# Kernel tuning notes

Measured on AMD Instinct MI355X. Metric: run time of the kernel, lower is better.

Reference implementation:

```python
import jax, jax.numpy as jnp
import numpy as np

WS = 8          # window size
HEADS = 3       # num_heads
DIM = 48        # channels


def _rel_pos_log(ws):
    # log-spaced relative coordinates, (N, N, 2) with N = ws*ws
    coords = jnp.stack(jnp.meshgrid(jnp.arange(ws), jnp.arange(ws), indexing='ij'))  # (2, ws, ws)
    cf = coords.reshape(2, -1)                                  # (2, N)
    rel = (cf[:, :, None] - cf[:, None, :]).transpose(1, 2, 0)  # (N, N, 2)
    rel = rel.astype(jnp.float32)
    return jnp.sign(rel) * jnp.log1p(jnp.abs(rel))


def setup_inputs() -> dict:
    key = jax.random.key(0)
    ks = jax.random.split(key, 11)
    s = 0.05  # keep pre-softmax logits in a sane range
    return {
        'X': jax.random.normal(ks[0], (2, DIM, 512, 512), jnp.float32),
        'v_w': jax.random.normal(ks[1], (DIM, DIM), jnp.float32) * s,
        'v_b': jnp.zeros((DIM,), jnp.float32),
        'qk_w': jax.random.normal(ks[2], (2 * DIM, DIM), jnp.float32) * s,
        'qk_b': jnp.zeros((2 * DIM,), jnp.float32),
        'proj_w': jax.random.normal(ks[3], (DIM, DIM), jnp.float32) * s,
        'proj_b': jnp.zeros((DIM,), jnp.float32),
        'meta1_w': jax.random.normal(ks[4], (256, 2), jnp.float32) * s,
        'meta1_b': jnp.zeros((256,), jnp.float32),
        'meta2_w': jax.random.normal(ks[5], (HEADS, 256), jnp.float32) * s,
        'meta2_b': jnp.zeros((HEADS,), jnp.float32),
    }


def _conv1x1(x, w, b):
    # x: [B, Cin, H, W], w: [Cout, Cin], b: [Cout]
    return jnp.einsum('oc,bchw->bohw', w, x) + b[None, :, None, None]


def reference(X, v_w, v_b, qk_w, qk_b, proj_w, proj_b,
              meta1_w, meta1_b, meta2_w, meta2_b):
    B, C, H, W = X.shape
    hd = C // HEADS
    scale = hd ** -0.5
    N = WS * WS

    V = _conv1x1(X, v_w, v_b)              # [B, C, H, W]
    QK = _conv1x1(X, qk_w, qk_b)           # [B, 2C, H, W]
    QKV = jnp.concatenate([QK, V], axis=1)  # [B, 3C, H, W]

    # window partition (shift=0, H/W multiples of WS -> no padding)
    nh, nw = H // WS, W // WS
    x = QKV.transpose(0, 2, 3, 1)                           # [B, H, W, 3C]
    x = x.reshape(B, nh, WS, nw, WS, 3 * C)
    x = x.transpose(0, 1, 3, 2, 4, 5).reshape(B * nh * nw, N, 3 * C)

    qkv = x.reshape(-1, N, 3, HEADS, hd).transpose(2, 0, 3, 1, 4)  # [3, B_, h, N, d]
    q, k, v = qkv[0], qkv[1], qkv[2]

    attn = jnp.einsum('bhnd,bhmd->bhnm', q * scale, k)       # [B_, h, N, N]

    # MLP relative position bias
    rel = _rel_pos_log(WS)                                   # [N, N, 2]
    hidden = jax.nn.relu(rel @ meta1_w.T + meta1_b)          # [N, N, 256]
    bias = (hidden @ meta2_w.T + meta2_b).transpose(2, 0, 1)  # [h, N, N]

    attn = jax.nn.softmax(attn + bias[None], axis=-1)
    out = jnp.einsum('bhnm,bhmd->bhnd', attn, v)             # [B_, h, N, d]
    out = out.transpose(0, 2, 1, 3).reshape(B * nh * nw, N, C)

    # window reverse
    out = out.reshape(B, nh, nw, WS, WS, C)
    out = out.transpose(0, 1, 3, 2, 4, 5).reshape(B, H, W, C)
    out = out.transpose(0, 3, 1, 2)                          # [B, C, H, W]

    return _conv1x1(out, proj_w, proj_b)
```

## Files before the change

### kernel.cpp

```cpp
#include <hip/hip_runtime.h>
#include <math.h>


typedef _Float16 f16x4 __attribute__((ext_vector_type(4)));
typedef float    f32x4 __attribute__((ext_vector_type(4)));

#define WS_BFRAG 0
#define WS_WFRAG 49152
#define WS_PFRAG 62976
#define WS_QKVB  67584
#define WS_PBIAS 68160

#define XT_S 52
#define T_S  100
#define VD_S 68

__global__ __launch_bounds__(256) void prep_kernel(
    const float* __restrict__ m1w, const float* __restrict__ m1b,
    const float* __restrict__ m2w, const float* __restrict__ m2b,
    const float* __restrict__ qk_w, const float* __restrict__ v_w,
    const float* __restrict__ proj_w,
    const float* __restrict__ qk_b, const float* __restrict__ v_b,
    const float* __restrict__ proj_b,
    unsigned char* __restrict__ ws)
{
    __shared__ float sm[1536];

    float*     bfrag = (float*)(ws + WS_BFRAG);
    _Float16*  wfrag = (_Float16*)(ws + WS_WFRAG);
    _Float16*  pfrag = (_Float16*)(ws + WS_PFRAG);
    float*     qkvb  = (float*)(ws + WS_QKVB);
    float*     pbias = (float*)(ws + WS_PBIAS);

    const int gid = blockIdx.x * 256 + threadIdx.x;
    if (blockIdx.x < 16) {
        for (int i = threadIdx.x; i < 1536; i += 256) {
            float v;
            if (i < 512)      v = m1w[i];
            else if (i < 768) v = m1b[i - 512];
            else              v = m2w[i - 768];
            sm[i] = v;
        }
        __syncthreads();

        const int n = gid >> 6, m = gid & 63;
        float di = (float)((n >> 3) - (m >> 3));
        float dj = (float)((n & 7) - (m & 7));
        float r0 = copysignf(log1pf(fabsf(di)), di);
        float r1 = copysignf(log1pf(fabsf(dj)), dj);
        float a0 = 0.f, a1 = 0.f, a2 = 0.f;
        #pragma unroll 4
        for (int k = 0; k < 256; ++k) {
            float hv = fmaxf(sm[512 + k] + sm[2*k]*r0 + sm[2*k+1]*r1, 0.f);
            a0 += sm[768 + k]  * hv;
            a1 += sm[1024 + k] * hv;
            a2 += sm[1280 + k] * hv;
        }
        const int tm = m >> 4, quad = (m >> 2) & 3, r = m & 3, tn = n >> 4;
        const int ln = quad*16 + (n & 15);
        const int base = ((tm*4 + tn)*64 + ln)*4 + r;
        bfrag[(0*16*64)*4  + base] = a0 + m2b[0];
        bfrag[(16*64)*4    + base] = a1 + m2b[1];
        bfrag[(32*64)*4    + base] = a2 + m2b[2];
    } else if (gid < 4096 + 6912) {
        const int idx = gid - 4096;
        const int j = idx & 3, l = (idx >> 2) & 63, f = idx >> 8;
        const int ks = f % 3, mt = f / 3;
        const int row = mt*16 + (l & 15), col = ks*16 + ((l >> 4) << 2) + j;
        const float wv = (row < 96) ? qk_w[row*48 + col] : v_w[(row-96)*48 + col];
        wfrag[idx] = (_Float16)wv;
    } else if (gid < 11008 + 2304) {
        const int idx = gid - 11008;
        const int j = idx & 3, l = (idx >> 2) & 63, f = idx >> 8;
        const int ks = f % 3, mt = f / 3;
        const int row = mt*16 + (l & 15), col = ks*16 + ((l >> 4) << 2) + j;
        pfrag[idx] = (_Float16)proj_w[row*48 + col];
    } else if (gid < 13312 + 144) {
        const int c = gid - 13312;
        qkvb[c] = (c < 96) ? qk_b[c] : v_b[c - 96];
    } else if (gid < 13456 + 48) {
        pbias[gid - 13456] = proj_b[gid - 13456];
    }
}

__global__ __launch_bounds__(256, 4) void win_attn_kernel(
    const float* __restrict__ X, const unsigned char* __restrict__ ws,
    float* __restrict__ out, int nblk)
{
    __shared__ _Float16 smem[12992];
    _Float16* sXO = smem;
    _Float16* sT  = smem + 64*XT_S;
    _Float16* sVd = smem + 64*XT_S + 64*T_S;

    const float* bfrag = (const float*)(ws + WS_BFRAG);
    const f16x4* wfrag = (const f16x4*)(ws + WS_WFRAG);
    const f16x4* pfrag = (const f16x4*)(ws + WS_PFRAG);
    const float* qkvb  = (const float*)(ws + WS_QKVB);
    const float* pbias = (const float*)(ws + WS_PBIAS);

    const int tid  = threadIdx.x;
    const int wave = tid >> 6, lane = tid & 63;
    const int lq   = lane >> 4, lm = lane & 15;

    const int blk = blockIdx.x;
    const int wid = (blk & 7) * (nblk >> 3) + (blk >> 3);
    const int batch = wid >> 12;
    const int wh = (wid >> 6) & 63, ww = wid & 63;
    const int h0 = wh << 3, w0 = ww << 3;

    const float* Xb = X + ((size_t)batch * 48 << 18);

    f32x4 xv[3];
    #pragma unroll
    for (int g = 0; g < 3; ++g) {
        const int f = tid*12 + g*4;
        const int c = f >> 6, rw = (f >> 3) & 7, cl = f & 7;
        xv[g] = *(const f32x4*)(Xb + ((size_t)c << 18) + (size_t)(h0 + rw)*512 + (w0 + cl));
    }
    f16x4 aw[27];
    #pragma unroll
    for (int fi = 0; fi < 27; ++fi) aw[fi] = wfrag[fi*64 + lane];
    #pragma unroll
    for (int g = 0; g < 3; ++g) {
        const int f = tid*12 + g*4;
        const int c = f >> 6, rw = (f >> 3) & 7, cl = f & 7;
        #pragma unroll
        for (int j = 0; j < 4; ++j)
            sXO[(rw*8 + cl + j)*XT_S + c] = (_Float16)xv[g][j];
    }
    __syncthreads();

    {
        f16x4 bx[3];
        #pragma unroll
        for (int ks = 0; ks < 3; ++ks)
            bx[ks] = *(const f16x4*)&sXO[(wave*16 + lm)*XT_S + ks*16 + lq*4];

        const int tok = wave*16 + lm;
        #pragma unroll
        for (int mt = 0; mt < 9; ++mt) {
            f32x4 acc = *(const f32x4*)&qkvb[mt*16 + lq*4];
            #pragma unroll
            for (int ks = 0; ks < 3; ++ks)
                acc = __builtin_amdgcn_mfma_f32_16x16x16f16(aw[mt*3+ks], bx[ks], acc, 0, 0, 0);
            if (mt < 3) {
                f16x4 hv;
                #pragma unroll
                for (int r = 0; r < 4; ++r) hv[r] = (_Float16)(acc[r] * 0.25f);
                *(f16x4*)&sT[tok*T_S + mt*16 + lq*4] = hv;
            } else if (mt < 6) {
                f16x4 hv;
                #pragma unroll
                for (int r = 0; r < 4; ++r) hv[r] = (_Float16)acc[r];
                *(f16x4*)&sT[tok*T_S + mt*16 + lq*4] = hv;
            } else {
                #pragma unroll
                for (int r = 0; r < 4; ++r)
                    sVd[((mt-6)*16 + lq*4 + r)*VD_S + tok] = (_Float16)acc[r];
            }
        }
    }

    const int tn = wave;
    f32x4 sb[3][4];
    #pragma unroll
    for (int h = 0; h < 3; ++h)
        #pragma unroll
        for (int tm = 0; tm < 4; ++tm)
            sb[h][tm] = ((const f32x4*)bfrag)[(h*16 + tm*4 + tn)*64 + lane];
    __syncthreads();

    #pragma unroll
    for (int h = 0; h < 3; ++h) {
        f16x4 ak[4];
        #pragma unroll
        for (int tm = 0; tm < 4; ++tm)
            ak[tm] = *(const f16x4*)&sT[(tm*16 + lm)*T_S + 48 + h*16 + lq*4];
        f16x4 bq = *(const f16x4*)&sT[(tn*16 + lm)*T_S + h*16 + lq*4];
        f32x4 s[4];
        #pragma unroll
        for (int tm = 0; tm < 4; ++tm)
            s[tm] = __builtin_amdgcn_mfma_f32_16x16x16f16(ak[tm], bq, sb[h][tm], 0, 0, 0);

        float sum = 0.f;
        #pragma unroll
        for (int tm = 0; tm < 4; ++tm)
            #pragma unroll
            for (int r = 0; r < 4; ++r) {
                float e = __expf(s[tm][r]);
                s[tm][r] = e; sum += e;
            }
        sum += __shfl_xor(sum, 16);
        sum += __shfl_xor(sum, 32);
        const float rinv = __builtin_amdgcn_rcpf(sum);

        f32x4 o = {0.f, 0.f, 0.f, 0.f};
        #pragma unroll
        for (int tm = 0; tm < 4; ++tm) {
            f16x4 av = *(const f16x4*)&sVd[(h*16 + lm)*VD_S + tm*16 + lq*4];
            f16x4 pf;
            pf[0] = (_Float16)s[tm][0];
            pf[1] = (_Float16)s[tm][1];
            pf[2] = (_Float16)s[tm][2];
            pf[3] = (_Float16)s[tm][3];
            o = __builtin_amdgcn_mfma_f32_16x16x16f16(av, pf, o, 0, 0, 0);
        }
        f16x4 hv;
        #pragma unroll
        for (int r = 0; r < 4; ++r) hv[r] = (_Float16)(o[r] * rinv);
        *(f16x4*)&sXO[(tn*16 + lm)*XT_S + h*16 + lq*4] = hv;
    }

    {
        f16x4 bo[3];
        #pragma unroll
        for (int ks = 0; ks < 3; ++ks)
            bo[ks] = *(const f16x4*)&sXO[(wave*16 + lm)*XT_S + ks*16 + lq*4];
        f16x4 ap[9];
        #pragma unroll
        for (int fi = 0; fi < 9; ++fi) ap[fi] = pfrag[fi*64 + lane];

        const int tok = wave*16 + lm;
        float* ob = out + ((size_t)batch * 48 << 18);
        const size_t pix = (size_t)(h0 + (tok >> 3)) * 512 + (w0 + (tok & 7));
        #pragma unroll
        for (int mt = 0; mt < 3; ++mt) {
            f32x4 acc = *(const f32x4*)&pbias[mt*16 + lq*4];
            #pragma unroll
            for (int ks = 0; ks < 3; ++ks)
                acc = __builtin_amdgcn_mfma_f32_16x16x16f16(ap[mt*3+ks], bo[ks], acc, 0, 0, 0);
            #pragma unroll
            for (int r = 0; r < 4; ++r)
                ob[((size_t)(mt*16 + lq*4 + r) << 18) + pix] = acc[r];
        }
    }
}

extern "C" void kernel_launch(void* const* d_in, const int* in_sizes, int n_in,
                              void* d_out, int out_size, void* d_ws, size_t ws_size,
                              hipStream_t stream) {
    (void)n_in; (void)out_size; (void)ws_size;
    const float* X      = (const float*)d_in[0];
    const float* v_w    = (const float*)d_in[1];
    const float* v_b    = (const float*)d_in[2];
    const float* qk_w   = (const float*)d_in[3];
    const float* qk_b   = (const float*)d_in[4];
    const float* proj_w = (const float*)d_in[5];
    const float* proj_b = (const float*)d_in[6];
    const float* m1w    = (const float*)d_in[7];
    const float* m1b    = (const float*)d_in[8];
    const float* m2w    = (const float*)d_in[9];
    const float* m2b    = (const float*)d_in[10];
    float* out = (float*)d_out;
    unsigned char* ws = (unsigned char*)d_ws;

    const int B = in_sizes[0] / (48 * 512 * 512);
    const int nblk = B * 64 * 64;

    hipLaunchKernelGGL(prep_kernel, dim3(53), dim3(256), 0, stream,
                       m1w, m1b, m2w, m2b, qk_w, v_w, proj_w, qk_b, v_b, proj_b, ws);
    hipLaunchKernelGGL(win_attn_kernel, dim3(nblk), dim3(256), 0, stream,
                       X, ws, out, nblk);
}
```

Measured before the change: 282.3 us.

## Cut registers and LDS to double occupancy, keep Q in registers, use exp2

Raises the occupancy target from 4 to 8 blocks per CU. It stops prefetching the weight, projection and bias fragments into registers and loads them from global memory at each MFMA instead. Q now stays in registers rather than LDS, so the LDS tile drops to K only and the shared footprint shrinks. The X load becomes scalar per-channel gathers with tokens across lanes, and log2e is folded into the bias and Q scale so the softmax can use exp2. The extra global or cache reads and the loss of load/compute overlap from prefetching could offset the gain from higher occupancy.

After: 284.0 us. About the same (+0.6%).

```diff
diff --git a/kernel.cpp b/kernel.cpp
--- a/kernel.cpp
+++ b/kernel.cpp
@@ -4,6 +4,8 @@
 
 typedef _Float16 f16x4 __attribute__((ext_vector_type(4)));
 typedef float    f32x4 __attribute__((ext_vector_type(4)));
+
+#define LOG2E 1.44269504f
 
 #define WS_BFRAG 0
 #define WS_WFRAG 49152
@@ -12,7 +14,7 @@
 #define WS_PBIAS 68160
 
 #define XT_S 52
-#define T_S  100
+#define K_S  52
 #define VD_S 68
 
 __global__ __launch_bounds__(256) void prep_kernel(
@@ -59,9 +61,9 @@
         const int tm = m >> 4, quad = (m >> 2) & 3, r = m & 3, tn = n >> 4;
         const int ln = quad*16 + (n & 15);
         const int base = ((tm*4 + tn)*64 + ln)*4 + r;
-        bfrag[(0*16*64)*4  + base] = a0 + m2b[0];
-        bfrag[(16*64)*4    + base] = a1 + m2b[1];
-        bfrag[(32*64)*4    + base] = a2 + m2b[2];
+        bfrag[(0*16*64)*4  + base] = (a0 + m2b[0]) * LOG2E;
+        bfrag[(16*64)*4    + base] = (a1 + m2b[1]) * LOG2E;
+        bfrag[(32*64)*4    + base] = (a2 + m2b[2]) * LOG2E;
     } else if (gid < 4096 + 6912) {
         const int idx = gid - 4096;
         const int j = idx & 3, l = (idx >> 2) & 63, f = idx >> 8;
@@ -83,14 +85,14 @@
     }
 }
 
-__global__ __launch_bounds__(256, 4) void win_attn_kernel(
+__global__ __launch_bounds__(256, 8) void win_attn_kernel(
     const float* __restrict__ X, const unsigned char* __restrict__ ws,
     float* __restrict__ out, int nblk)
 {
-    __shared__ _Float16 smem[12992];
+    __shared__ _Float16 smem[9920];
     _Float16* sXO = smem;
-    _Float16* sT  = smem + 64*XT_S;
-    _Float16* sVd = smem + 64*XT_S + 64*T_S;
+    _Float16* sK  = smem + 64*XT_S;
+    _Float16* sVd = smem + 64*XT_S + 64*K_S;
 
     const float* bfrag = (const float*)(ws + WS_BFRAG);
     const f16x4* wfrag = (const f16x4*)(ws + WS_WFRAG);
@@ -110,26 +112,18 @@
 
     const float* Xb = X + ((size_t)batch * 48 << 18);
 
-    f32x4 xv[3];
-    #pragma unroll
-    for (int g = 0; g < 3; ++g) {
-        const int f = tid*12 + g*4;
-        const int c = f >> 6, rw = (f >> 3) & 7, cl = f & 7;
-        xv[g] = *(const f32x4*)(Xb + ((size_t)c << 18) + (size_t)(h0 + rw)*512 + (w0 + cl));
-    }
-    f16x4 aw[27];
-    #pragma unroll
-    for (int fi = 0; fi < 27; ++fi) aw[fi] = wfrag[fi*64 + lane];
-    #pragma unroll
-    for (int g = 0; g < 3; ++g) {
-        const int f = tid*12 + g*4;
-        const int c = f >> 6, rw = (f >> 3) & 7, cl = f & 7;
-        #pragma unroll
-        for (int j = 0; j < 4; ++j)
-            sXO[(rw*8 + cl + j)*XT_S + c] = (_Float16)xv[g][j];
+    {
+        const int tok = lane;
+        const size_t pix = (size_t)(h0 + (tok >> 3)) * 512 + (w0 + (tok & 7));
+        #pragma unroll
+        for (int k = 0; k < 12; ++k) {
+            const int c = wave + (k << 2);
+            sXO[tok*XT_S + c] = (_Float16)Xb[((size_t)c << 18) + pix];
+        }
     }
     __syncthreads();
 
+    f16x4 qf[3];
     {
         f16x4 bx[3];
         #pragma unroll
@@ -142,17 +136,17 @@
             f32x4 acc = *(const f32x4*)&qkvb[mt*16 + lq*4];
             #pragma unroll
             for (int ks = 0; ks < 3; ++ks)
-                acc = __builtin_amdgcn_mfma_f32_16x16x16f16(aw[mt*3+ks], bx[ks], acc, 0, 0, 0);
+                acc = __builtin_amdgcn_mfma_f32_16x16x16f16(
+                          wfrag[(mt*3+ks)*64 + lane], bx[ks], acc, 0, 0, 0);
             if (mt < 3) {
-                f16x4 hv;
                 #pragma unroll
-                for (int r = 0; r < 4; ++r) hv[r] = (_Float16)(acc[r] * 0.25f);
-                *(f16x4*)&sT[tok*T_S + mt*16 + lq*4] = hv;
+                for (int r = 0; r < 4; ++r)
+                    qf[mt][r] = (_Float16)(acc[r] * (0.25f * LOG2E));
             } else if (mt < 6) {
                 f16x4 hv;
                 #pragma unroll
                 for (int r = 0; r < 4; ++r) hv[r] = (_Float16)acc[r];
-                *(f16x4*)&sT[tok*T_S + mt*16 + lq*4] = hv;
+                *(f16x4*)&sK[tok*K_S + (mt-3)*16 + lq*4] = hv;
             } else {
                 #pragma unroll
                 for (int r = 0; r < 4; ++r)
@@ -160,34 +154,28 @@
             }
         }
     }
+    __syncthreads();
 
     const int tn = wave;
-    f32x4 sb[3][4];
-    #pragma unroll
-    for (int h = 0; h < 3; ++h)
-        #pragma unroll
-        for (int tm = 0; tm < 4; ++tm)
-            sb[h][tm] = ((const f32x4*)bfrag)[(h*16 + tm*4 + tn)*64 + lane];
-    __syncthreads();
-
+    const f32x4* bf = (const f32x4*)bfrag;
     #pragma unroll
     for (int h = 0; h < 3; ++h) {
         f16x4 ak[4];
         #pragma unroll
         for (int tm = 0; tm < 4; ++tm)
-            ak[tm] = *(const f16x4*)&sT[(tm*16 + lm)*T_S + 48 + h*16 + lq*4];
-        f16x4 bq = *(const f16x4*)&sT[(tn*16 + lm)*T_S + h*16 + lq*4];
+            ak[tm] = *(const f16x4*)&sK[(tm*16 + lm)*K_S + h*16 + lq*4];
         f32x4 s[4];
         #pragma unroll
         for (int tm = 0; tm < 4; ++tm)
-            s[tm] = __builtin_amdgcn_mfma_f32_16x16x16f16(ak[tm], bq, sb[h][tm], 0, 0, 0);
+            s[tm] = __builtin_amdgcn_mfma_f32_16x16x16f16(
+                        ak[tm], qf[h], bf[(h*16 + tm*4 + tn)*64 + lane], 0, 0, 0);
 
         float sum = 0.f;
         #pragma unroll
         for (int tm = 0; tm < 4; ++tm)
             #pragma unroll
             for (int r = 0; r < 4; ++r) {
-                float e = __expf(s[tm][r]);
+                float e = __builtin_amdgcn_exp2f(s[tm][r]);
                 s[tm][r] = e; sum += e;
             }
         sum += __shfl_xor(sum, 16);
@@ -216,9 +204,6 @@
         #pragma unroll
         for (int ks = 0; ks < 3; ++ks)
             bo[ks] = *(const f16x4*)&sXO[(wave*16 + lm)*XT_S + ks*16 + lq*4];
-        f16x4 ap[9];
-        #pragma unroll
-        for (int fi = 0; fi < 9; ++fi) ap[fi] = pfrag[fi*64 + lane];
 
         const int tok = wave*16 + lm;
         float* ob = out + ((size_t)batch * 48 << 18);
@@ -228,7 +213,8 @@
             f32x4 acc = *(const f32x4*)&pbias[mt*16 + lq*4];
             #pragma unroll
             for (int ks = 0; ks < 3; ++ks)
-                acc = __builtin_amdgcn_mfma_f32_16x16x16f16(ap[mt*3+ks], bo[ks], acc, 0, 0, 0);
+                acc = __builtin_amdgcn_mfma_f32_16x16x16f16(
+                          pfrag[(mt*3+ks)*64 + lane], bo[ks], acc, 0, 0, 0);
             #pragma unroll
             for (int r = 0; r < 4; ++r)
                 ob[((size_t)(mt*16 + lq*4 + r) << 18) + pix] = acc[r];
```
